# Kernel optimization log

Hardware: AMD Instinct MI355X
Metric: run time of the kernel (lower is better)

Reference implementation:

```python
import jax, jax.numpy as jnp
import numpy as np

S, B, D, H, V = 1024, 4, 1024, 4096, 32000
EPS = 1e-5

def _ln(x, g, b):
    m = jnp.mean(x, axis=-1, keepdims=True)
    v = jnp.var(x, axis=-1, keepdims=True)
    return (x - m) * jax.lax.rsqrt(v + EPS) * g + b

def setup_inputs() -> dict:
    key = jax.random.key(0)
    ks = jax.random.split(key, 12)
    def xav(k, shape):
        fan_in, fan_out = shape[1], shape[0]
        lim = np.sqrt(6.0 / (fan_in + fan_out))
        return jax.random.uniform(k, shape, jnp.float32, -lim, lim)
    return {
        "inputs": jax.random.randint(ks[0], (S, B), 0, V, dtype=jnp.int32),
        "emb_table": jax.random.normal(ks[1], (V, D), jnp.float32),
        "WQ": xav(ks[2], (D, D)),
        "WK": xav(ks[3], (D, D)),
        "WV": xav(ks[4], (D, D)),
        "Wo": xav(ks[5], (D, D)),
        "bo": jnp.zeros((D,), jnp.float32),
        "W1": xav(ks[6], (H, D)),
        "b1": jnp.zeros((H,), jnp.float32),
        "W2": xav(ks[7], (D, H)),
        "b2": jnp.zeros((D,), jnp.float32),
        "g1": jnp.ones((D,), jnp.float32),
        "be1": jnp.zeros((D,), jnp.float32),
        "g2": jnp.ones((D,), jnp.float32),
        "be2": jnp.zeros((D,), jnp.float32),
        "Wd": xav(ks[8], (V, D)),
        "bd": jnp.zeros((V,), jnp.float32),
    }

def reference(inputs, emb_table, WQ, WK, WV, Wo, bo, W1, b1, W2, b2, g1, be1, g2, be2, Wd, bd):
    # inputs: [S, B] int ids
    emb = emb_table[inputs]                       # [S, B, D]
    # F.linear(x, W) == x @ W.T
    Q = jnp.einsum('sbd,ed->bse', emb, WQ)        # [B, S, D]
    K = jnp.einsum('sbd,ed->bse', emb, WK)
    Vv = jnp.einsum('sbd,ed->bse', emb, WV)
    scores = jnp.einsum('bqd,bkd->bqk', Q, K) / jnp.sqrt(jnp.float32(D))
    attn = jax.nn.softmax(scores, axis=-1)        # [B, S, S]
    z = jnp.einsum('bqk,bkd->qbd', attn, Vv)      # back to [S, B, D]
    z = jnp.einsum('sbd,ed->sbe', z, Wo) + bo
    x = _ln(emb + z, g1, be1)
    ffn = jnp.einsum('sbh,dh->sbd', jax.nn.relu(jnp.einsum('sbd,hd->sbh', x, W1) + b1), W2) + b2
    out = _ln(x + ffn, g2, be2)
    logits = out.reshape(S * B, D) @ Wd.T + bd    # [S*B, V]
    return logits
```

## Files before the change

### kernel.cpp

```cpp
#include <hip/hip_runtime.h>

typedef float f32x4 __attribute__((ext_vector_type(4)));
typedef __bf16 bf16x8 __attribute__((ext_vector_type(8)));
typedef int i32x4 __attribute__((ext_vector_type(4)));
typedef unsigned short u16;
typedef unsigned short u16x4 __attribute__((ext_vector_type(4)));
typedef unsigned short u16x8 __attribute__((ext_vector_type(8)));
typedef unsigned int u32;

#define SEQ 1024
#define NBATCH 4
#define DM 1024
#define HD 4096
#define NV 32000
#define NT (SEQ * NBATCH)

__device__ __forceinline__ u16 f2bf(float f) {
  u32 u = __builtin_bit_cast(u32, f);
  return (u16)((u + 0x7FFFu + ((u >> 16) & 1u)) >> 16);
}

__global__ __launch_bounds__(256) void cast_bf16_kernel(const float* __restrict__ in,
                                                        u16* __restrict__ out, int n8) {
  int i = blockIdx.x * 256 + threadIdx.x;
  if (i >= n8) return;
  const f32x4* p = (const f32x4*)(in + (long)i * 8);
  f32x4 a = p[0], b = p[1];
  u16x8 o;
  o[0] = f2bf(a[0]); o[1] = f2bf(a[1]); o[2] = f2bf(a[2]); o[3] = f2bf(a[3]);
  o[4] = f2bf(b[0]); o[5] = f2bf(b[1]); o[6] = f2bf(b[2]); o[7] = f2bf(b[3]);
  *(u16x8*)(out + (long)i * 8) = o;
}

__global__ __launch_bounds__(256) void embed_kernel(const int* __restrict__ ids,
                                                    const float* __restrict__ tab,
                                                    float* __restrict__ ef,
                                                    u16* __restrict__ eh) {
  int t = blockIdx.x, tid = threadIdx.x;
  long id = ids[t];
  f32x4 v = *(const f32x4*)(tab + id * DM + tid * 4);
  *(f32x4*)(ef + (long)t * DM + tid * 4) = v;
  u16x4 h;
  h[0] = f2bf(v[0]); h[1] = f2bf(v[1]); h[2] = f2bf(v[2]); h[3] = f2bf(v[3]);
  *(u16x4*)(eh + (long)t * DM + tid * 4) = h;
}

__global__ __launch_bounds__(256) void softmax_kernel(const float* __restrict__ s,
                                                      u16* __restrict__ p) {
  int row = blockIdx.x, tid = threadIdx.x;
  const float* rp = s + (long)row * SEQ;
  f32x4 v = *(const f32x4*)(rp + tid * 4);
  float mx = fmaxf(fmaxf(v[0], v[1]), fmaxf(v[2], v[3]));
  for (int o = 32; o; o >>= 1) mx = fmaxf(mx, __shfl_xor(mx, o));
  __shared__ float red[4];
  if ((tid & 63) == 0) red[tid >> 6] = mx;
  __syncthreads();
  mx = fmaxf(fmaxf(red[0], red[1]), fmaxf(red[2], red[3]));
  const float sc = 0.03125f;
  f32x4 e;
  e[0] = expf((v[0] - mx) * sc); e[1] = expf((v[1] - mx) * sc);
  e[2] = expf((v[2] - mx) * sc); e[3] = expf((v[3] - mx) * sc);
  float sm = e[0] + e[1] + e[2] + e[3];
  for (int o = 32; o; o >>= 1) sm += __shfl_xor(sm, o);
  __syncthreads();
  if ((tid & 63) == 0) red[tid >> 6] = sm;
  __syncthreads();
  sm = red[0] + red[1] + red[2] + red[3];
  float inv = 1.0f / sm;
  u16x4 o4;
  o4[0] = f2bf(e[0] * inv); o4[1] = f2bf(e[1] * inv);
  o4[2] = f2bf(e[2] * inv); o4[3] = f2bf(e[3] * inv);
  *(u16x4*)(p + (long)row * SEQ + tid * 4) = o4;
}

__global__ __launch_bounds__(256) void ln_kernel(const float* __restrict__ in,
                                                 const float* __restrict__ g,
                                                 const float* __restrict__ be,
                                                 float* __restrict__ outf,
                                                 u16* __restrict__ outh) {
  int row = blockIdx.x, tid = threadIdx.x;
  f32x4 v = *(const f32x4*)(in + (long)row * DM + tid * 4);
  float s = v[0] + v[1] + v[2] + v[3];
  float q = v[0] * v[0] + v[1] * v[1] + v[2] * v[2] + v[3] * v[3];
  for (int o = 32; o; o >>= 1) { s += __shfl_xor(s, o); q += __shfl_xor(q, o); }
  __shared__ float rs_[4], rq_[4];
  if ((tid & 63) == 0) { rs_[tid >> 6] = s; rq_[tid >> 6] = q; }
  __syncthreads();
  s = rs_[0] + rs_[1] + rs_[2] + rs_[3];
  q = rq_[0] + rq_[1] + rq_[2] + rq_[3];
  float mean = s * (1.0f / DM);
  float var = q * (1.0f / DM) - mean * mean;
  float rstd = rsqrtf(var + 1e-5f);
  f32x4 gg = *(const f32x4*)(g + tid * 4);
  f32x4 bb = *(const f32x4*)(be + tid * 4);
  f32x4 y;
  y[0] = (v[0] - mean) * rstd * gg[0] + bb[0];
  y[1] = (v[1] - mean) * rstd * gg[1] + bb[1];
  y[2] = (v[2] - mean) * rstd * gg[2] + bb[2];
  y[3] = (v[3] - mean) * rstd * gg[3] + bb[3];
  if (outf) *(f32x4*)(outf + (long)row * DM + tid * 4) = y;
  if (outh) {
    u16x4 h;
    h[0] = f2bf(y[0]); h[1] = f2bf(y[1]); h[2] = f2bf(y[2]); h[3] = f2bf(y[3]);
    *(u16x4*)(outh + (long)row * DM + tid * 4) = h;
  }
}

__global__ __launch_bounds__(256) void ln_i8_kernel(const float* __restrict__ in,
                                                    const float* __restrict__ g,
                                                    const float* __restrict__ be,
                                                    char* __restrict__ q8,
                                                    float* __restrict__ scale) {
  int row = blockIdx.x, tid = threadIdx.x;
  f32x4 v = *(const f32x4*)(in + (long)row * DM + tid * 4);
  float s = v[0] + v[1] + v[2] + v[3];
  float q = v[0] * v[0] + v[1] * v[1] + v[2] * v[2] + v[3] * v[3];
  for (int o = 32; o; o >>= 1) { s += __shfl_xor(s, o); q += __shfl_xor(q, o); }
  __shared__ float rs_[4], rq_[4], rm_[4];
  if ((tid & 63) == 0) { rs_[tid >> 6] = s; rq_[tid >> 6] = q; }
  __syncthreads();
  s = rs_[0] + rs_[1] + rs_[2] + rs_[3];
  q = rq_[0] + rq_[1] + rq_[2] + rq_[3];
  float mean = s * (1.0f / DM);
  float var = q * (1.0f / DM) - mean * mean;
  float rstd = rsqrtf(var + 1e-5f);
  f32x4 gg = *(const f32x4*)(g + tid * 4);
  f32x4 bb = *(const f32x4*)(be + tid * 4);
  f32x4 y;
  y[0] = (v[0] - mean) * rstd * gg[0] + bb[0];
  y[1] = (v[1] - mean) * rstd * gg[1] + bb[1];
  y[2] = (v[2] - mean) * rstd * gg[2] + bb[2];
  y[3] = (v[3] - mean) * rstd * gg[3] + bb[3];
  float am = fmaxf(fmaxf(fabsf(y[0]), fabsf(y[1])), fmaxf(fabsf(y[2]), fabsf(y[3])));
  for (int o = 32; o; o >>= 1) am = fmaxf(am, __shfl_xor(am, o));
  __syncthreads();
  if ((tid & 63) == 0) rm_[tid >> 6] = am;
  __syncthreads();
  am = fmaxf(fmaxf(rm_[0], rm_[1]), fmaxf(rm_[2], rm_[3]));
  float inv = (am > 0.f) ? 127.f / am : 0.f;
  int q0 = (int)rintf(y[0] * inv), q1 = (int)rintf(y[1] * inv);
  int q2 = (int)rintf(y[2] * inv), q3 = (int)rintf(y[3] * inv);
  u32 pk = (q0 & 255) | ((q1 & 255) << 8) | ((q2 & 255) << 16) | ((u32)(q3 & 255) << 24);
  *(u32*)(q8 + (size_t)row * DM + tid * 4) = pk;
  if (tid == 0) scale[row] = am * (1.0f / 127.f);
}

__global__ __launch_bounds__(256) void rowq_i8_kernel(const float* __restrict__ in,
                                                      char* __restrict__ q8,
                                                      float* __restrict__ scale) {
  int row = blockIdx.x, tid = threadIdx.x;
  f32x4 v = *(const f32x4*)(in + (size_t)row * DM + tid * 4);
  float am = fmaxf(fmaxf(fabsf(v[0]), fabsf(v[1])), fmaxf(fabsf(v[2]), fabsf(v[3])));
  for (int o = 32; o; o >>= 1) am = fmaxf(am, __shfl_xor(am, o));
  __shared__ float rm_[4];
  if ((tid & 63) == 0) rm_[tid >> 6] = am;
  __syncthreads();
  am = fmaxf(fmaxf(rm_[0], rm_[1]), fmaxf(rm_[2], rm_[3]));
  float inv = (am > 0.f) ? 127.f / am : 0.f;
  int q0 = (int)rintf(v[0] * inv), q1 = (int)rintf(v[1] * inv);
  int q2 = (int)rintf(v[2] * inv), q3 = (int)rintf(v[3] * inv);
  u32 pk = (q0 & 255) | ((q1 & 255) << 8) | ((q2 & 255) << 16) | ((u32)(q3 & 255) << 24);
  *(u32*)(q8 + (size_t)row * DM + tid * 4) = pk;
  if (tid == 0) scale[row] = am * (1.0f / 127.f);
}

#define GLD(gp, lp)                                              \
  __builtin_amdgcn_global_load_lds(                              \
      (__attribute__((address_space(1))) void*)(gp),             \
      (__attribute__((address_space(3))) void*)(lp), 16, 0, 0)

#define BM 128
#define BN 128
#define BK 32

__global__ __launch_bounds__(256) void gemm_bt(
    const u16* __restrict__ A, const u16* __restrict__ B,
    float* __restrict__ Cf, u16* __restrict__ Ch,
    const float* __restrict__ bias, const float* __restrict__ resid,
    int K, int lda, int ldb, int ldc,
    long batA, long batB, long batC, int relu) {
  __shared__ u16 As[BM * BK];
  __shared__ u16 Bs[BN * BK];
  const int tid = threadIdx.x;
  const int bz = blockIdx.z;
  A += (long)bz * batA;
  B += (long)bz * batB;
  const long cbase = (long)bz * batC;
  const int row0 = blockIdx.y * BM;
  const int col0 = blockIdx.x * BN;
  const int l = tid & 63;
  const int w = tid >> 6;
  const int wr = (w >> 1) * 64, wc = (w & 1) * 64;

  f32x4 acc[4][4] = {};

  const u16* gA = A + (long)(row0 + (tid >> 2)) * lda + (tid & 3) * 8;
  const u16* gB = B + (long)(col0 + (tid >> 2)) * ldb + (tid & 3) * 8;
  const long a64 = (long)64 * lda, b64 = (long)64 * ldb;
  u16* lA = As + tid * 8;
  u16* lB = Bs + tid * 8;

  const int fr = l & 15;
  const int fk = (l >> 4) * 8;
  const u16* rA = As + (wr + fr) * BK + fk;
  const u16* rB = Bs + (wc + fr) * BK + fk;

  for (int k0 = 0; k0 < K; k0 += BK) {
    GLD(gA + k0, lA);
    GLD(gA + a64 + k0, lA + 2048);
    GLD(gB + k0, lB);
    GLD(gB + b64 + k0, lB + 2048);
    __syncthreads();
    bf16x8 af[4], bf[4];
#pragma unroll
    for (int m = 0; m < 4; ++m) af[m] = *(const bf16x8*)(rA + m * 16 * BK);
#pragma unroll
    for (int n = 0; n < 4; ++n) bf[n] = *(const bf16x8*)(rB + n * 16 * BK);
#pragma unroll
    for (int m = 0; m < 4; ++m)
#pragma unroll
      for (int n = 0; n < 4; ++n)
        acc[m][n] = __builtin_amdgcn_mfma_f32_16x16x32_bf16(af[m], bf[n], acc[m][n], 0, 0, 0);
    __syncthreads();
  }

  const int er = row0 + wr + ((l >> 4) << 2);
  const int ec = col0 + wc + (l & 15);
#pragma unroll
  for (int m = 0; m < 4; ++m) {
#pragma unroll
    for (int n = 0; n < 4; ++n) {
      f32x4 v = acc[m][n];
      const int c = ec + n * 16;
      float bv = bias ? bias[c] : 0.0f;
#pragma unroll
      for (int i = 0; i < 4; ++i) {
        const int r = er + m * 16 + i;
        float x = v[i] + bv;
        if (resid) x += resid[(long)r * ldc + c];
        if (relu) x = fmaxf(x, 0.0f);
        if (Cf) Cf[cbase + (long)r * ldc + c] = x;
        if (Ch) Ch[cbase + (long)r * ldc + c] = f2bf(x);
      }
    }
  }
}

__global__ __launch_bounds__(256) void gemm_i8(
    const char* __restrict__ A, const char* __restrict__ B,
    float* __restrict__ C, const float* __restrict__ sA, const float* __restrict__ sB,
    const float* __restrict__ bias, int K, int lda, int ldb, int ldc,
    int Mtiles, int Ntiles) {
  __shared__ __align__(16) char As[128 * 64];
  __shared__ __align__(16) char Bs[128 * 64];
  const int tid = threadIdx.x;

  const int nwg = gridDim.x;
  const int blk = blockIdx.x;
  const int cpx = nwg >> 3;
  const int wg = (blk & 7) * cpx + (blk >> 3);
  const int gsz = 4 * Ntiles;
  const int gid = wg / gsz;
  const int rem = wg - gid * gsz;
  const int row0 = (gid * 4 + (rem & 3)) * 128;
  const int col0 = (rem >> 2) * 128;

  const int l = tid & 63;
  const int w = tid >> 6;
  const int wr = (w >> 1) * 64, wc = (w & 1) * 64;

  const int srow = tid >> 2;
  const int sslot = (tid & 3) ^ ((srow >> 1) & 3);
  const char* gA = A + (size_t)(row0 + srow) * lda + sslot * 16;
  const char* gB = B + (size_t)(col0 + srow) * ldb + sslot * 16;
  const size_t a64 = (size_t)64 * lda, b64 = (size_t)64 * ldb;
  char* lA = As + tid * 16;
  char* lB = Bs + tid * 16;

  const int fr = l & 15;
  const int fsw = 16 * ((l >> 4) ^ ((fr >> 1) & 3));
  const char* rA = As + (wr + fr) * 64 + fsw;
  const char* rB = Bs + (wc + fr) * 64 + fsw;

  i32x4 acc[4][4] = {};

  for (int k0 = 0; k0 < K; k0 += 64) {
    GLD(gA + k0, lA);
    GLD(gA + a64 + k0, lA + 4096);
    GLD(gB + k0, lB);
    GLD(gB + b64 + k0, lB + 4096);
    __syncthreads();
    i32x4 af[4], bf[4];
#pragma unroll
    for (int m = 0; m < 4; ++m) af[m] = *(const i32x4*)(rA + m * 16 * 64);
#pragma unroll
    for (int n = 0; n < 4; ++n) bf[n] = *(const i32x4*)(rB + n * 16 * 64);
#pragma unroll
    for (int m = 0; m < 4; ++m)
#pragma unroll
      for (int n = 0; n < 4; ++n)
        acc[m][n] = __builtin_amdgcn_mfma_i32_16x16x64_i8(af[m], bf[n], acc[m][n], 0, 0, 0);
    __syncthreads();
  }

  const int er = row0 + wr + ((l >> 4) << 2);
  const int ec = col0 + wc + (l & 15);
#pragma unroll
  for (int m = 0; m < 4; ++m) {
#pragma unroll
    for (int n = 0; n < 4; ++n) {
      i32x4 v = acc[m][n];
      const int c = ec + n * 16;
      const float sb = sB[c];
      const float bv = bias ? bias[c] : 0.0f;
#pragma unroll
      for (int i = 0; i < 4; ++i) {
        const int r = er + m * 16 + i;
        C[(size_t)r * ldc + c] = (float)v[i] * (sA[r] * sb) + bv;
      }
    }
  }
}

#define DSB() __builtin_amdgcn_sched_barrier(0)
#define SBAR() __builtin_amdgcn_s_barrier()

template <int N0, int N1>
__device__ __forceinline__ void mfma16(f32x4 (&acc)[8][4], const bf16x8 (&af)[8],
                                       bf16x8 b0, bf16x8 b1) {
#pragma unroll
  for (int m = 0; m < 8; ++m) {
    acc[m][N0] = __builtin_amdgcn_mfma_f32_16x16x32_bf16(af[m], b0, acc[m][N0], 0, 0, 0);
    acc[m][N1] = __builtin_amdgcn_mfma_f32_16x16x32_bf16(af[m], b1, acc[m][N1], 0, 0, 0);
  }
}

__global__ __launch_bounds__(512, 2) void gemm256_bt(
    const u16* __restrict__ A, const u16* __restrict__ B,
    float* __restrict__ Cf, u16* __restrict__ Ch,
    const float* __restrict__ bias,
    int K, int lda, int ldb, int ldc, int Mtiles, int Ntiles, int relu) {
  __shared__ __align__(16) u16 As[2][2][128 * 64];
  __shared__ __align__(16) u16 Bs[2][2][256 * 32];
  const int tid = threadIdx.x;

  const int nwg = gridDim.x;
  const int blk = blockIdx.x;
  const int cpx = nwg >> 3;
  const int wg = (blk & 7) * cpx + (blk >> 3);
  const int gsz = 4 * Ntiles;
  const int gid = wg / gsz;
  const int rem = wg - gid * gsz;
  const int row0 = (gid * 4 + (rem & 3)) * 256;
  const int col0 = (rem >> 2) * 256;

  const int l = tid & 63;
  const int w = tid >> 6;
  const int wr = w >> 2;
  const int wc = w & 3;

  const int sArow = tid >> 3;
  const int sAcol = ((tid & 7) ^ ((sArow >> 1) & 7)) * 8;
  const int sBrow = tid >> 2;
  const int sBcol = ((tid & 3) ^ ((sBrow >> 2) & 3)) * 8;

  const u16* gA = A + (size_t)(row0 + sArow) * lda + sAcol;
  const u16* gB = B + (size_t)(col0 + sBrow) * ldb + sBcol;
  const size_t a64 = (size_t)64 * lda;
  const size_t b128 = (size_t)128 * ldb;

#define STAGE_A(buf, h, kt)                                          \
  do {                                                               \
    const u16* _g = gA + (size_t)(h) * 128 * lda + (size_t)(kt) * 64;\
    u16* _l = &As[buf][h][0] + tid * 8;                              \
    GLD(_g, _l);                                                     \
    GLD(_g + a64, _l + 4096);                                        \
  } while (0)
#define STAGE_B(buf, kk, kt)                                         \
  do {                                                               \
    const u16* _g = gB + (size_t)(kt) * 64 + (kk) * 32;              \
    u16* _l = &Bs[buf][kk][0] + tid * 8;                             \
    GLD(_g, _l);                                                     \
    GLD(_g + b128, _l + 4096);                                       \
  } while (0)

  const int fr = l & 15;
  const int g8 = (l >> 4) * 8;
  const int acp0 = g8 ^ (((fr >> 1) & 7) * 8);
  const int acp1 = (32 + g8) ^ (((fr >> 1) & 7) * 8);
  const int bcp = g8 ^ (((fr >> 2) & 3) * 8);

#define RA(buf, m, cp) (*(const bf16x8*)(&As[buf][wr][((m) * 16 + fr) * 64 + (cp)]))
#define RB(buf, n, kk) (*(const bf16x8*)(&Bs[buf][kk][(wc * 64 + (n) * 16 + fr) * 32 + bcp]))

  f32x4 acc[8][4] = {};
  bf16x8 a0[8], a1[8], bb0, bb1;

  const int nkt = K >> 6;
  const int nit = nkt >> 1;

  STAGE_A(0, 0, 0); STAGE_A(0, 1, 0);
  STAGE_B(0, 0, 0); STAGE_B(0, 1, 0);
  STAGE_B(1, 0, 1); STAGE_A(1, 0, 1);
  asm volatile("s_waitcnt vmcnt(4)"); DSB();
  SBAR();

  for (int i = 0; i < nit; ++i) {
    const int u = 2 * i + 1;
    const int v = (2 * i + 2 < nkt) ? 2 * i + 2 : nkt - 1;
    const int w2 = (2 * i + 3 < nkt) ? 2 * i + 3 : nkt - 1;

#pragma unroll
    for (int m = 0; m < 8; ++m) a0[m] = RA(0, m, acp0);
    bb0 = RB(0, 0, 0); bb1 = RB(0, 1, 0);
    STAGE_A(1, 1, u);
    SBAR();
    asm volatile("s_waitcnt lgkmcnt(0)"); DSB();
    __builtin_amdgcn_s_setprio(1);
    mfma16<0, 1>(acc, a0, bb0, bb1);
    __builtin_amdgcn_s_setprio(0);
    SBAR();
    bb0 = RB(0, 2, 0); bb1 = RB(0, 3, 0);
    STAGE_B(1, 1, u);
    asm volatile("s_waitcnt vmcnt(6)"); DSB();
    SBAR();
    asm volatile("s_waitcnt lgkmcnt(0)"); DSB();
    __builtin_amdgcn_s_setprio(1);
    mfma16<2, 3>(acc, a0, bb0, bb1);
    __builtin_amdgcn_s_setprio(0);
    SBAR();
#pragma unroll
    for (int m = 0; m < 8; ++m) a1[m] = RA(0, m, acp1);
    bb0 = RB(0, 0, 1); bb1 = RB(0, 1, 1);
    STAGE_B(0, 0, v);
    SBAR();
    asm volatile("s_waitcnt lgkmcnt(0)"); DSB();
    __builtin_amdgcn_s_setprio(1);
    mfma16<0, 1>(acc, a1, bb0, bb1);
    __builtin_amdgcn_s_setprio(0);
    SBAR();
    bb0 = RB(0, 2, 1); bb1 = RB(0, 3, 1);
    STAGE_A(0, 0, v);
    asm volatile("s_waitcnt vmcnt(6)"); DSB();
    SBAR();
    asm volatile("s_waitcnt lgkmcnt(0)"); DSB();
    __builtin_amdgcn_s_setprio(1);
    mfma16<2, 3>(acc, a1, bb0, bb1);
    __builtin_amdgcn_s_setprio(0);
    SBAR();
#pragma unroll
    for (int m = 0; m < 8; ++m) a0[m] = RA(1, m, acp0);
    bb0 = RB(1, 0, 0); bb1 = RB(1, 1, 0);
    STAGE_A(0, 1, v);
    SBAR();
    asm volatile("s_waitcnt lgkmcnt(0)"); DSB();
    __builtin_amdgcn_s_setprio(1);
    mfma16<0, 1>(acc, a0, bb0, bb1);
    __builtin_amdgcn_s_setprio(0);
    SBAR();
    bb0 = RB(1, 2, 0); bb1 = RB(1, 3, 0);
    STAGE_B(0, 1, v);
    asm volatile("s_waitcnt vmcnt(6)"); DSB();
    SBAR();
    asm volatile("s_waitcnt lgkmcnt(0)"); DSB();
    __builtin_amdgcn_s_setprio(1);
    mfma16<2, 3>(acc, a0, bb0, bb1);
    __builtin_amdgcn_s_setprio(0);
    SBAR();
#pragma unroll
    for (int m = 0; m < 8; ++m) a1[m] = RA(1, m, acp1);
    bb0 = RB(1, 0, 1); bb1 = RB(1, 1, 1);
    STAGE_B(1, 0, w2);
    SBAR();
    asm volatile("s_waitcnt lgkmcnt(0)"); DSB();
    __builtin_amdgcn_s_setprio(1);
    mfma16<0, 1>(acc, a1, bb0, bb1);
    __builtin_amdgcn_s_setprio(0);
    SBAR();
    bb0 = RB(1, 2, 1); bb1 = RB(1, 3, 1);
    STAGE_A(1, 0, w2);
    asm volatile("s_waitcnt vmcnt(6)"); DSB();
    SBAR();
    asm volatile("s_waitcnt lgkmcnt(0)"); DSB();
    __builtin_amdgcn_s_setprio(1);
    mfma16<2, 3>(acc, a1, bb0, bb1);
    __builtin_amdgcn_s_setprio(0);
    SBAR();
  }

  asm volatile("s_waitcnt vmcnt(0)"); DSB();

  const int er = row0 + wr * 128 + ((l >> 4) << 2);
  const int ec = col0 + wc * 64 + (l & 15);
#pragma unroll
  for (int m = 0; m < 8; ++m) {
#pragma unroll
    for (int n = 0; n < 4; ++n) {
      f32x4 vv = acc[m][n];
      const int c = ec + n * 16;
      float bv = bias ? bias[c] : 0.0f;
#pragma unroll
      for (int i = 0; i < 4; ++i) {
        const int r = er + m * 16 + i;
        float x = vv[i] + bv;
        if (relu) x = fmaxf(x, 0.0f);
        if (Cf) Cf[(size_t)r * ldc + c] = x;
        if (Ch) Ch[(size_t)r * ldc + c] = f2bf(x);
      }
    }
  }
#undef STAGE_A
#undef STAGE_B
#undef RA
#undef RB
}

extern "C" void kernel_launch(void* const* d_in, const int* in_sizes, int n_in,
                              void* d_out, int out_size, void* d_ws, size_t ws_size,
                              hipStream_t stream) {
  const int* ids = (const int*)d_in[0];
  const float* tab = (const float*)d_in[1];
  const float* WQ = (const float*)d_in[2];
  const float* WK = (const float*)d_in[3];
  const float* WV = (const float*)d_in[4];
  const float* Wo = (const float*)d_in[5];
  const float* bo = (const float*)d_in[6];
  const float* W1 = (const float*)d_in[7];
  const float* b1 = (const float*)d_in[8];
  const float* W2 = (const float*)d_in[9];
  const float* b2 = (const float*)d_in[10];
  const float* g1 = (const float*)d_in[11];
  const float* be1 = (const float*)d_in[12];
  const float* g2 = (const float*)d_in[13];
  const float* be2 = (const float*)d_in[14];
  const float* Wd = (const float*)d_in[15];
  const float* bd = (const float*)d_in[16];
  float* logits = (float*)d_out;

  if (ws_size < 280000000ull) return;

  char* p = (char*)d_ws;
  auto alloc = [&](size_t bytes) {
    char* r = p;
    p += (bytes + 255) & ~(size_t)255;
    return r;
  };
  float* embf = (float*)alloc((size_t)NT * DM * 4);
  u16* embh = (u16*)alloc((size_t)NT * DM * 2);
  u16* WQh = (u16*)alloc((size_t)DM * DM * 2);
  u16* WKh = (u16*)alloc((size_t)DM * DM * 2);
  u16* WVh = (u16*)alloc((size_t)DM * DM * 2);
  u16* Woh = (u16*)alloc((size_t)DM * DM * 2);
  u16* W1h = (u16*)alloc((size_t)HD * DM * 2);
  u16* W2h = (u16*)alloc((size_t)DM * HD * 2);
  char* Wdq = (char*)alloc((size_t)NV * DM);
  float* sWd = (float*)alloc((size_t)NV * 4);
  u16* Qh = (u16*)alloc((size_t)NT * DM * 2);
  u16* Kh = (u16*)alloc((size_t)NT * DM * 2);
  u16* VTh = (u16*)alloc((size_t)NBATCH * DM * SEQ * 2);
  float* scoresf = (float*)alloc((size_t)NBATCH * SEQ * SEQ * 4);
  u16* Ph = (u16*)alloc((size_t)NBATCH * SEQ * SEQ * 2);
  u16* zh = (u16*)alloc((size_t)NT * DM * 2);
  float* r1f = (float*)alloc((size_t)NT * DM * 4);
  float* xf = (float*)alloc((size_t)NT * DM * 4);
  u16* xh = (u16*)alloc((size_t)NT * DM * 2);
  u16* hh = (u16*)alloc((size_t)NT * HD * 2);
  float* r2f = (float*)alloc((size_t)NT * DM * 4);
  char* outq = (char*)alloc((size_t)NT * DM);
  float* sOut = (float*)alloc((size_t)NT * 4);

  cast_bf16_kernel<<<dim3(DM * DM / 8 / 256), 256, 0, stream>>>(WQ, WQh, DM * DM / 8);
  cast_bf16_kernel<<<dim3(DM * DM / 8 / 256), 256, 0, stream>>>(WK, WKh, DM * DM / 8);
  cast_bf16_kernel<<<dim3(DM * DM / 8 / 256), 256, 0, stream>>>(WV, WVh, DM * DM / 8);
  cast_bf16_kernel<<<dim3(DM * DM / 8 / 256), 256, 0, stream>>>(Wo, Woh, DM * DM / 8);
  cast_bf16_kernel<<<dim3(HD * DM / 8 / 256), 256, 0, stream>>>(W1, W1h, HD * DM / 8);
  cast_bf16_kernel<<<dim3(DM * HD / 8 / 256), 256, 0, stream>>>(W2, W2h, DM * HD / 8);
  rowq_i8_kernel<<<dim3(NV), 256, 0, stream>>>(Wd, Wdq, sWd);

  embed_kernel<<<NT, 256, 0, stream>>>(ids, tab, embf, embh);

  gemm_bt<<<dim3(DM / BN, NT / BM, 1), 256, 0, stream>>>(
      embh, WQh, nullptr, Qh, nullptr, nullptr, DM, DM, DM, DM, 0, 0, 0, 0);
  gemm_bt<<<dim3(DM / BN, NT / BM, 1), 256, 0, stream>>>(
      embh, WKh, nullptr, Kh, nullptr, nullptr, DM, DM, DM, DM, 0, 0, 0, 0);

  gemm_bt<<<dim3(SEQ / BN, DM / BM, NBATCH), 256, 0, stream>>>(
      WVh, embh, nullptr, VTh, nullptr, nullptr, DM, DM, NBATCH * DM, SEQ,
      0, DM, (long)DM * SEQ, 0);

  gemm_bt<<<dim3(SEQ / BN, SEQ / BM, NBATCH), 256, 0, stream>>>(
      Qh, Kh, scoresf, nullptr, nullptr, nullptr, DM, NBATCH * DM, NBATCH * DM, SEQ,
      DM, DM, (long)SEQ * SEQ, 0);

  softmax_kernel<<<NBATCH * SEQ, 256, 0, stream>>>(scoresf, Ph);

  gemm_bt<<<dim3(DM / BN, SEQ / BM, NBATCH), 256, 0, stream>>>(
      Ph, VTh, nullptr, zh, nullptr, nullptr, SEQ, SEQ, SEQ, NBATCH * DM,
      (long)SEQ * SEQ, (long)DM * SEQ, DM, 0);

  gemm_bt<<<dim3(DM / BN, NT / BM, 1), 256, 0, stream>>>(
      zh, Woh, r1f, nullptr, bo, embf, DM, DM, DM, DM, 0, 0, 0, 0);

  ln_kernel<<<NT, 256, 0, stream>>>(r1f, g1, be1, xf, xh);

  gemm256_bt<<<dim3((NT / 256) * (HD / 256)), 512, 0, stream>>>(
      xh, W1h, nullptr, hh, b1, DM, DM, DM, HD, NT / 256, HD / 256, 1);
  gemm_bt<<<dim3(DM / BN, NT / BM, 1), 256, 0, stream>>>(
      hh, W2h, r2f, nullptr, b2, xf, HD, HD, HD, DM, 0, 0, 0, 0);

  ln_i8_kernel<<<NT, 256, 0, stream>>>(r2f, g2, be2, outq, sOut);

  gemm_i8<<<dim3((NT / 128) * (NV / 128)), 256, 0, stream>>>(
      outq, Wdq, logits, sOut, sWd, bd, DM, DM, DM, NV, NT / 128, NV / 128);
}
```

Measured before the change: 794.5 us.

## Double-buffer int8 logits GEMM, fuse Q/K projections, nontemporal logits stores

The int8 logits GEMM now uses two LDS buffers, so the global-to-LDS load of the next K tile is issued before the MFMAs on the current tile, with one barrier per tile instead of two. Its output stores become nontemporal to avoid polluting the cache with the large logits matrix. The Q and K projection weights are packed into one buffer and computed in a single wider GEMM, with the scores GEMM reading Q and K through adjusted strides. Risks: doubled LDS use may lower occupancy, and the loop assumes the number of K tiles is even.

Result: faster. 756.7 us (-4.8%).

```diff
diff --git a/kernel.cpp b/kernel.cpp
--- a/kernel.cpp
+++ b/kernel.cpp
@@ -246,13 +246,16 @@
   }
 }
 
+#define DSB() __builtin_amdgcn_sched_barrier(0)
+#define SBAR() __builtin_amdgcn_s_barrier()
+
 __global__ __launch_bounds__(256) void gemm_i8(
     const char* __restrict__ A, const char* __restrict__ B,
     float* __restrict__ C, const float* __restrict__ sA, const float* __restrict__ sB,
     const float* __restrict__ bias, int K, int lda, int ldb, int ldc,
     int Mtiles, int Ntiles) {
-  __shared__ __align__(16) char As[128 * 64];
-  __shared__ __align__(16) char Bs[128 * 64];
+  __shared__ __align__(16) char As[2][128 * 64];
+  __shared__ __align__(16) char Bs[2][128 * 64];
   const int tid = threadIdx.x;
 
   const int nwg = gridDim.x;
@@ -274,33 +277,53 @@
   const char* gA = A + (size_t)(row0 + srow) * lda + sslot * 16;
   const char* gB = B + (size_t)(col0 + srow) * ldb + sslot * 16;
   const size_t a64 = (size_t)64 * lda, b64 = (size_t)64 * ldb;
-  char* lA = As + tid * 16;
-  char* lB = Bs + tid * 16;
+
+#define STAGE_I8(buf, kt)                                            \
+  do {                                                               \
+    const char* _ga = gA + (size_t)(kt) * 64;                        \
+    const char* _gb = gB + (size_t)(kt) * 64;                        \
+    GLD(_ga, &As[buf][0] + tid * 16);                                \
+    GLD(_ga + a64, &As[buf][4096] + tid * 16);                       \
+    GLD(_gb, &Bs[buf][0] + tid * 16);                                \
+    GLD(_gb + b64, &Bs[buf][4096] + tid * 16);                       \
+  } while (0)
 
   const int fr = l & 15;
   const int fsw = 16 * ((l >> 4) ^ ((fr >> 1) & 3));
-  const char* rA = As + (wr + fr) * 64 + fsw;
-  const char* rB = Bs + (wc + fr) * 64 + fsw;
+  const int raoff = (wr + fr) * 64 + fsw;
+  const int rboff = (wc + fr) * 64 + fsw;
 
   i32x4 acc[4][4] = {};
 
-  for (int k0 = 0; k0 < K; k0 += 64) {
-    GLD(gA + k0, lA);
-    GLD(gA + a64 + k0, lA + 4096);
-    GLD(gB + k0, lB);
-    GLD(gB + b64 + k0, lB + 4096);
-    __syncthreads();
-    i32x4 af[4], bf[4];
-#pragma unroll
-    for (int m = 0; m < 4; ++m) af[m] = *(const i32x4*)(rA + m * 16 * 64);
-#pragma unroll
-    for (int n = 0; n < 4; ++n) bf[n] = *(const i32x4*)(rB + n * 16 * 64);
-#pragma unroll
-    for (int m = 0; m < 4; ++m)
-#pragma unroll
-      for (int n = 0; n < 4; ++n)
-        acc[m][n] = __builtin_amdgcn_mfma_i32_16x16x64_i8(af[m], bf[n], acc[m][n], 0, 0, 0);
-    __syncthreads();
+#define COMPUTE_I8(buf)                                                         \
+  do {                                                                          \
+    i32x4 af[4], bf[4];                                                         \
+    _Pragma("unroll")                                                           \
+    for (int m = 0; m < 4; ++m) af[m] = *(const i32x4*)(&As[buf][raoff + m * 1024]); \
+    _Pragma("unroll")                                                           \
+    for (int n = 0; n < 4; ++n) bf[n] = *(const i32x4*)(&Bs[buf][rboff + n * 1024]); \
+    _Pragma("unroll")                                                           \
+    for (int m = 0; m < 4; ++m)                                                 \
+      _Pragma("unroll")                                                         \
+      for (int n = 0; n < 4; ++n)                                               \
+        acc[m][n] = __builtin_amdgcn_mfma_i32_16x16x64_i8(af[m], bf[n], acc[m][n], 0, 0, 0); \
+  } while (0)
+
+  const int nkt = K >> 6;
+
+  STAGE_I8(0, 0);
+  asm volatile("s_waitcnt vmcnt(0)"); DSB();
+  SBAR();
+
+  for (int t = 0; t < nkt; t += 2) {
+    STAGE_I8(1, t + 1);
+    COMPUTE_I8(0);
+    asm volatile("s_waitcnt vmcnt(0)"); DSB();
+    SBAR();
+    if (t + 2 < nkt) STAGE_I8(0, t + 2);
+    COMPUTE_I8(1);
+    asm volatile("s_waitcnt vmcnt(0)"); DSB();
+    SBAR();
   }
 
   const int er = row0 + wr + ((l >> 4) << 2);
@@ -316,14 +339,14 @@
 #pragma unroll
       for (int i = 0; i < 4; ++i) {
         const int r = er + m * 16 + i;
-        C[(size_t)r * ldc + c] = (float)v[i] * (sA[r] * sb) + bv;
+        __builtin_nontemporal_store((float)v[i] * (sA[r] * sb) + bv,
+                                    &C[(size_t)r * ldc + c]);
       }
     }
   }
-}
-
-#define DSB() __builtin_amdgcn_sched_barrier(0)
-#define SBAR() __builtin_amdgcn_s_barrier()
+#undef STAGE_I8
+#undef COMPUTE_I8
+}
 
 template <int N0, int N1>
 __device__ __forceinline__ void mfma16(f32x4 (&acc)[8][4], const bf16x8 (&af)[8],
@@ -547,16 +570,14 @@
   };
   float* embf = (float*)alloc((size_t)NT * DM * 4);
   u16* embh = (u16*)alloc((size_t)NT * DM * 2);
-  u16* WQh = (u16*)alloc((size_t)DM * DM * 2);
-  u16* WKh = (u16*)alloc((size_t)DM * DM * 2);
+  u16* WQKh = (u16*)alloc((size_t)2 * DM * DM * 2);
   u16* WVh = (u16*)alloc((size_t)DM * DM * 2);
   u16* Woh = (u16*)alloc((size_t)DM * DM * 2);
   u16* W1h = (u16*)alloc((size_t)HD * DM * 2);
   u16* W2h = (u16*)alloc((size_t)DM * HD * 2);
   char* Wdq = (char*)alloc((size_t)NV * DM);
   float* sWd = (float*)alloc((size_t)NV * 4);
-  u16* Qh = (u16*)alloc((size_t)NT * DM * 2);
-  u16* Kh = (u16*)alloc((size_t)NT * DM * 2);
+  u16* QKh = (u16*)alloc((size_t)NT * 2 * DM * 2);
   u16* VTh = (u16*)alloc((size_t)NBATCH * DM * SEQ * 2);
   float* scoresf = (float*)alloc((size_t)NBATCH * SEQ * SEQ * 4);
   u16* Ph = (u16*)alloc((size_t)NBATCH * SEQ * SEQ * 2);
@@ -569,8 +590,8 @@
   char* outq = (char*)alloc((size_t)NT * DM);
   float* sOut = (float*)alloc((size_t)NT * 4);
 
-  cast_bf16_kernel<<<dim3(DM * DM / 8 / 256), 256, 0, stream>>>(WQ, WQh, DM * DM / 8);
-  cast_bf16_kernel<<<dim3(DM * DM / 8 / 256), 256, 0, stream>>>(WK, WKh, DM * DM / 8);
+  cast_bf16_kernel<<<dim3(DM * DM / 8 / 256), 256, 0, stream>>>(WQ, WQKh, DM * DM / 8);
+  cast_bf16_kernel<<<dim3(DM * DM / 8 / 256), 256, 0, stream>>>(WK, WQKh + (size_t)DM * DM, DM * DM / 8);
   cast_bf16_kernel<<<dim3(DM * DM / 8 / 256), 256, 0, stream>>>(WV, WVh, DM * DM / 8);
   cast_bf16_kernel<<<dim3(DM * DM / 8 / 256), 256, 0, stream>>>(Wo, Woh, DM * DM / 8);
   cast_bf16_kernel<<<dim3(HD * DM / 8 / 256), 256, 0, stream>>>(W1, W1h, HD * DM / 8);
@@ -579,18 +600,17 @@
 
   embed_kernel<<<NT, 256, 0, stream>>>(ids, tab, embf, embh);
 
-  gemm_bt<<<dim3(DM / BN, NT / BM, 1), 256, 0, stream>>>(
-      embh, WQh, nullptr, Qh, nullptr, nullptr, DM, DM, DM, DM, 0, 0, 0, 0);
-  gemm_bt<<<dim3(DM / BN, NT / BM, 1), 256, 0, stream>>>(
-      embh, WKh, nullptr, Kh, nullptr, nullptr, DM, DM, DM, DM, 0, 0, 0, 0);
+  gemm_bt<<<dim3(2 * DM / BN, NT / BM, 1), 256, 0, stream>>>(
+      embh, WQKh, nullptr, QKh, nullptr, nullptr, DM, DM, DM, 2 * DM, 0, 0, 0, 0);
 
   gemm_bt<<<dim3(SEQ / BN, DM / BM, NBATCH), 256, 0, stream>>>(
       WVh, embh, nullptr, VTh, nullptr, nullptr, DM, DM, NBATCH * DM, SEQ,
       0, DM, (long)DM * SEQ, 0);
 
   gemm_bt<<<dim3(SEQ / BN, SEQ / BM, NBATCH), 256, 0, stream>>>(
-      Qh, Kh, scoresf, nullptr, nullptr, nullptr, DM, NBATCH * DM, NBATCH * DM, SEQ,
-      DM, DM, (long)SEQ * SEQ, 0);
+      QKh, QKh + DM, scoresf, nullptr, nullptr, nullptr, DM,
+      NBATCH * 2 * DM, NBATCH * 2 * DM, SEQ,
+      2 * DM, 2 * DM, (long)SEQ * SEQ, 0);
 
   softmax_kernel<<<NBATCH * SEQ, 256, 0, stream>>>(scoresf, Ph);
 
```
